# Kernel tuning notes

Measured on AMD Instinct MI355X. Metric: run time of the kernel, lower is better.

## Reference

```python
import jax, jax.numpy as jnp
import numpy as np

EMBED_DIM = 768
NUM_HEADS = 12
HEAD_DIM = EMBED_DIM // NUM_HEADS
B, L = 1, 2048


def setup_inputs() -> dict:
    key = jax.random.key(0)
    ks = jax.random.split(key, 10)
    D = EMBED_DIM
    s = 1.0 / np.sqrt(D)
    x = jax.random.normal(ks[0], (B, L, D), dtype=jnp.float32)
    Wq = jax.random.uniform(ks[1], (D, D), jnp.float32, -s, s)
    bq = jax.random.uniform(ks[2], (D,), jnp.float32, -s, s)
    Wk = jax.random.uniform(ks[3], (D, D), jnp.float32, -s, s)
    bk = jax.random.uniform(ks[4], (D,), jnp.float32, -s, s)
    Wv = jax.random.uniform(ks[5], (D, D), jnp.float32, -s, s)
    bv = jax.random.uniform(ks[6], (D,), jnp.float32, -s, s)
    Wo = jax.random.uniform(ks[7], (D, D), jnp.float32, -s, s)
    bo = jax.random.uniform(ks[8], (D,), jnp.float32, -s, s)
    theta = jnp.zeros((1, NUM_HEADS, 1, 1), dtype=jnp.float32)
    return {"x": x, "Wq": Wq, "bq": bq, "Wk": Wk, "bk": bk,
            "Wv": Wv, "bv": bv, "Wo": Wo, "bo": bo, "theta": theta}


def _heads(t):
    # [B,L,D] -> [B,H,L,d_k]
    b, l, d = t.shape
    return t.reshape(b, l, NUM_HEADS, HEAD_DIM).transpose(0, 2, 1, 3)


def reference(x, Wq, bq, Wk, bk, Wv, bv, Wo, bo, theta):
    b, l, d = x.shape
    d_k = HEAD_DIM
    q = _heads(x @ Wq.T + bq)  # [B,H,L,dk]
    k = _heads(x @ Wk.T + bk)
    v = _heads(x @ Wv.T + bv)
    # squared pairwise L2 distance (== torch.cdist(q,k,p=2)**2), scaled by d_k
    qn = jnp.sum(q * q, axis=-1, keepdims=True)          # [B,H,L,1]
    kn = jnp.sum(k * k, axis=-1, keepdims=True)          # [B,H,L,1]
    qk = jnp.einsum('bhid,bhjd->bhij', q, k)             # [B,H,L,L]
    dist_sq = jnp.maximum(qn + kn.transpose(0, 1, 3, 2) - 2.0 * qk, 0.0) / d_k
    # global max over the full LxL matrix per (B,H)
    dist_max = jnp.max(dist_sq, axis=(-1, -2), keepdims=True)
    dist_norm = dist_sq / (dist_max + 1e-6)
    dsexp = jnp.exp(theta)                               # [1,H,1,1]
    attn_logits = jnp.exp(-dsexp * dist_norm)            # [B,H,L,L]
    attn_weights = jax.nn.softmax(attn_logits, axis=-1)
    context = jnp.einsum('bhij,bhjd->bhid', attn_weights, v)  # [B,H,L,dk]
    context = context.transpose(0, 2, 1, 3).reshape(b, l, d)
    output = context @ Wo.T + bo
    return output, attn_weights.mean(axis=1)
```

## Files before the change

kernel.cpp:

```cpp
#include <hip/hip_runtime.h>
#include <hip/hip_bf16.h>


typedef __bf16 bf16_t;
typedef bf16_t bf16x8 __attribute__((ext_vector_type(8)));
typedef bf16_t bf16x4 __attribute__((ext_vector_type(4)));
typedef float f32x4 __attribute__((ext_vector_type(4)));

#define L_SEQ 2048
#define DIM 768
#define NH 12
#define DKH 64
#define MDJ 4

__device__ __forceinline__ bf16x8 ldg8(const bf16_t* p) { return *(const bf16x8*)p; }
__device__ __forceinline__ f32x4 mfma16(bf16x8 a, bf16x8 b, f32x4 c_) {
  return __builtin_amdgcn_mfma_f32_16x16x32_bf16(a, b, c_, 0, 0, 0);
}


struct Tile2 { bf16x8 r[2]; };

__device__ __forceinline__ void tile_load(const bf16_t* __restrict__ src, int stride,
                                          Tile2& t_, int tid) {
#pragma unroll
  for (int c = 0; c < 2; ++c) {
    int chunk = tid + c * 256;
    t_.r[c] = *(const bf16x8*)&src[(size_t)(chunk >> 3) * stride + (chunk & 7) * 8];
  }
}

__device__ __forceinline__ void tile_write(bf16_t (*dst)[72], const Tile2& t_, int tid) {
#pragma unroll
  for (int c = 0; c < 2; ++c) {
    int chunk = tid + c * 256;
    *(bf16x8*)&dst[chunk >> 3][(chunk & 7) * 8] = t_.r[c];
  }
}

__device__ __forceinline__ void mfma_nt64(bf16_t (*As)[72], bf16_t (*Bs)[72],
                                          int wid, int lane, f32x4 acc[4]) {
#pragma unroll
  for (int ks = 0; ks < 2; ++ks) {
    bf16x8 a = *(const bf16x8*)&As[wid * 16 + (lane & 15)][ks * 32 + (lane >> 4) * 8];
#pragma unroll
    for (int nt = 0; nt < 4; ++nt) {
      bf16x8 b = *(const bf16x8*)&Bs[nt * 16 + (lane & 15)][ks * 32 + (lane >> 4) * 8];
      acc[nt] = mfma16(a, b, acc[nt]);
    }
  }
}


__global__ void cast_x(const float* __restrict__ in, bf16_t* __restrict__ out, int n4) {
  int i = blockIdx.x * 256 + threadIdx.x;
  if (i >= n4) return;
  float4 v = ((const float4*)in)[i];
  bf16_t* o = out + (size_t)i * 4;
  o[0] = (bf16_t)v.x; o[1] = (bf16_t)v.y; o[2] = (bf16_t)v.z; o[3] = (bf16_t)v.w;
}

__global__ void cast_w4(const float* __restrict__ w0, const float* __restrict__ w1,
                        const float* __restrict__ w2, const float* __restrict__ w3,
                        bf16_t* __restrict__ o0, bf16_t* __restrict__ o1,
                        bf16_t* __restrict__ o2, bf16_t* __restrict__ o3, int n4) {
  int i = blockIdx.x * 256 + threadIdx.x;
  if (i >= n4) return;
  const float* in = blockIdx.y == 0 ? w0 : blockIdx.y == 1 ? w1 : blockIdx.y == 2 ? w2 : w3;
  bf16_t* out = blockIdx.y == 0 ? o0 : blockIdx.y == 1 ? o1 : blockIdx.y == 2 ? o2 : o3;
  float4 v = ((const float4*)in)[i];
  bf16_t* o = out + (size_t)i * 4;
  o[0] = (bf16_t)v.x; o[1] = (bf16_t)v.y; o[2] = (bf16_t)v.z; o[3] = (bf16_t)v.w;
}


__global__ __launch_bounds__(256) void gemm_qkv(const bf16_t* __restrict__ x,
                                                const bf16_t* __restrict__ Bq,
                                                const bf16_t* __restrict__ Bk,
                                                const bf16_t* __restrict__ Bv,
                                                const float* __restrict__ bq,
                                                const float* __restrict__ bk,
                                                const float* __restrict__ bv,
                                                bf16_t* __restrict__ qo,
                                                bf16_t* __restrict__ ko,
                                                bf16_t* __restrict__ vto,
                                                float* __restrict__ qn,
                                                float* __restrict__ kn) {
  __shared__ bf16_t As[2][64][72];
  __shared__ bf16_t Bs[2][64][72];
  const int z = blockIdx.z;
  const bf16_t* B = z == 0 ? Bq : z == 1 ? Bk : Bv;
  const float* bias = z == 0 ? bq : z == 1 ? bk : bv;
  const int tid = threadIdx.x, wid = tid >> 6, lane = tid & 63;
  const int c = lane & 15, hi = lane >> 4;
  const int m0 = blockIdx.y * 64, n0 = blockIdx.x * 64;
  Tile2 at, bt;
  tile_load(x + (size_t)m0 * DIM, DIM, at, tid);
  tile_load(B + (size_t)n0 * DIM, DIM, bt, tid);
  f32x4 acc[4] = {};
  for (int kk = 0; kk < 12; ++kk) {
    tile_write(As[kk & 1], at, tid);
    tile_write(Bs[kk & 1], bt, tid);
    __syncthreads();
    if (kk < 11) {
      tile_load(x + (size_t)m0 * DIM + (kk + 1) * 64, DIM, at, tid);
      tile_load(B + (size_t)n0 * DIM + (kk + 1) * 64, DIM, bt, tid);
    }
    mfma_nt64(As[kk & 1], Bs[kk & 1], wid, lane, acc);
    __syncthreads();
  }
  const int r0 = wid * 16 + hi * 4;
  float ss[4] = {0.f, 0.f, 0.f, 0.f};
#pragma unroll
  for (int nt = 0; nt < 4; ++nt) {
    int cc = n0 + nt * 16 + c;
    float bv_ = bias[cc];
    int h = cc >> 6, d = cc & 63;
#pragma unroll
    for (int r = 0; r < 4; ++r) {
      int mm = m0 + r0 + r;
      float val = acc[nt][r] + bv_;
      if (z == 2) {
        vto[(size_t)cc * L_SEQ + mm] = (bf16_t)val;
      } else {
        bf16_t* out = z == 0 ? qo : ko;
        out[((size_t)h * L_SEQ + mm) * 64 + d] = (bf16_t)val;
        ss[r] = fmaf(val, val, ss[r]);
      }
    }
  }
  if (z < 2) {
#pragma unroll
    for (int s = 1; s < 16; s <<= 1)
#pragma unroll
      for (int r = 0; r < 4; ++r) ss[r] += __shfl_xor(ss[r], s);
    if (c == 0) {
      float* norm = z == 0 ? qn : kn;
      int h = n0 >> 6;
#pragma unroll
      for (int r = 0; r < 4; ++r) norm[h * L_SEQ + m0 + r0 + r] = ss[r];
    }
  }
}

__global__ __launch_bounds__(256) void gemm_out(const bf16_t* __restrict__ A,
                                                const bf16_t* __restrict__ B,
                                                const float* __restrict__ bias,
                                                float* __restrict__ out) {
  __shared__ bf16_t As[2][64][72];
  __shared__ bf16_t Bs[2][64][72];
  const int tid = threadIdx.x, wid = tid >> 6, lane = tid & 63;
  const int c = lane & 15, hi = lane >> 4;
  const int m0 = blockIdx.y * 64, n0 = blockIdx.x * 64;
  Tile2 at, bt;
  tile_load(A + (size_t)m0 * DIM, DIM, at, tid);
  tile_load(B + (size_t)n0 * DIM, DIM, bt, tid);
  f32x4 acc[4] = {};
  for (int kk = 0; kk < 12; ++kk) {
    tile_write(As[kk & 1], at, tid);
    tile_write(Bs[kk & 1], bt, tid);
    __syncthreads();
    if (kk < 11) {
      tile_load(A + (size_t)m0 * DIM + (kk + 1) * 64, DIM, at, tid);
      tile_load(B + (size_t)n0 * DIM + (kk + 1) * 64, DIM, bt, tid);
    }
    mfma_nt64(As[kk & 1], Bs[kk & 1], wid, lane, acc);
    __syncthreads();
  }
  const int r0 = wid * 16 + hi * 4;
#pragma unroll
  for (int nt = 0; nt < 4; ++nt) {
    int cc = n0 + nt * 16 + c;
    float bv = bias[cc];
#pragma unroll
    for (int r = 0; r < 4; ++r)
      out[(size_t)(m0 + r0 + r) * DIM + cc] = acc[nt][r] + bv;
  }
}


__global__ __launch_bounds__(256) void maxdist(const bf16_t* __restrict__ q,
                                               const bf16_t* __restrict__ k,
                                               const float* __restrict__ qn,
                                               const float* __restrict__ kn,
                                               float* __restrict__ blockmax) {
  __shared__ bf16_t Ks[2][64][72];
  __shared__ float wmax[4];
  const int it = blockIdx.x, jc = blockIdx.y, h = blockIdx.z;
  const int i0 = it * 64, jbase = jc * (L_SEQ / MDJ);
  const int tid = threadIdx.x, wid = tid >> 6, lane = tid & 63;
  const int c = lane & 15, hi = lane >> 4;
  bf16x8 qb[4][2];
  float aq[4];
#pragma unroll
  for (int nt = 0; nt < 4; ++nt) {
    const bf16_t* qr = q + ((size_t)h * L_SEQ + i0 + nt * 16 + c) * DKH;
    qb[nt][0] = ldg8(qr + hi * 8);
    qb[nt][1] = ldg8(qr + 32 + hi * 8);
    aq[nt] = qn[h * L_SEQ + i0 + nt * 16 + c];
  }
  Tile2 kt;
  tile_load(k + ((size_t)h * L_SEQ + jbase) * DKH, DKH, kt, tid);
  float m = 0.f;
  const int NT = L_SEQ / MDJ / 64;
  for (int t = 0; t < NT; ++t) {
    tile_write(Ks[t & 1], kt, tid);
    if (t < NT - 1)
      tile_load(k + ((size_t)h * L_SEQ + jbase + (t + 1) * 64) * DKH, DKH, kt, tid);
    __syncthreads();
    f32x4 acc[4] = {};
#pragma unroll
    for (int ks = 0; ks < 2; ++ks) {
      bf16x8 a = *(const bf16x8*)&Ks[t & 1][wid * 16 + c][ks * 32 + hi * 8];
#pragma unroll
      for (int nt = 0; nt < 4; ++nt) acc[nt] = mfma16(a, qb[nt][ks], acc[nt]);
    }
    f32x4 knj = *(const f32x4*)&kn[h * L_SEQ + jbase + t * 64 + wid * 16 + hi * 4];
#pragma unroll
    for (int nt = 0; nt < 4; ++nt)
#pragma unroll
      for (int r = 0; r < 4; ++r)
        m = fmaxf(m, fmaf(-2.f, acc[nt][r], aq[nt] + knj[r]));
  }
#pragma unroll
  for (int s = 1; s < 64; s <<= 1) m = fmaxf(m, __shfl_xor(m, s));
  if (lane == 0) wmax[wid] = m;
  __syncthreads();
  if (tid == 0) {
    float bm = fmaxf(fmaxf(wmax[0], wmax[1]), fmaxf(wmax[2], wmax[3]));
    blockmax[(h * MDJ + jc) * (L_SEQ / 64) + it] = fmaxf(bm, 0.f) * (1.f / 64.f);
  }
}

__global__ void reduce_dmax(const float* __restrict__ blockmax, float* __restrict__ dmax) {
  __shared__ float wm[2];
  const int h = blockIdx.x, tid = threadIdx.x, lane = tid & 63, wid = tid >> 6;
  float m = blockmax[h * 128 + tid];
#pragma unroll
  for (int s = 1; s < 64; s <<= 1) m = fmaxf(m, __shfl_xor(m, s));
  if (lane == 0) wm[wid] = m;
  __syncthreads();
  if (tid == 0) dmax[h] = fmaxf(wm[0], wm[1]);
}


__global__ __launch_bounds__(256) void fusedctx(const bf16_t* __restrict__ q,
                                                const bf16_t* __restrict__ k,
                                                const bf16_t* __restrict__ vt,
                                                const float* __restrict__ qn,
                                                const float* __restrict__ kn,
                                                const float* __restrict__ dmax,
                                                const float* __restrict__ theta,
                                                float* __restrict__ denP,
                                                float* __restrict__ ctxP, int JC) {
  __shared__ bf16_t Ks[2][64][72];
  __shared__ bf16_t Vs[2][64][72];
  __shared__ bf16_t Ws[64][72];
  __shared__ float denW[4][64];
  const int it = blockIdx.x, jc = blockIdx.y, h = blockIdx.z;
  const int i0 = it * 64;
  const int JLEN = L_SEQ / JC, jbase = jc * JLEN;
  const int tid = threadIdx.x, wid = tid >> 6, lane = tid & 63;
  const int c = lane & 15, hi = lane >> 4;
  const float sc = __expf(theta[h]) * (1.f / 64.f) / (dmax[h] + 1e-6f);
  const float twosc = 2.f * sc;
  bf16x8 qb[4][2];
  float naq[4];
#pragma unroll
  for (int nt = 0; nt < 4; ++nt) {
    const bf16_t* qr = q + ((size_t)h * L_SEQ + i0 + nt * 16 + c) * DKH;
    qb[nt][0] = ldg8(qr + hi * 8);
    qb[nt][1] = ldg8(qr + 32 + hi * 8);
    naq[nt] = -sc * qn[h * L_SEQ + i0 + nt * 16 + c];
  }
  Tile2 kt, vtr;
  tile_load(k + ((size_t)h * L_SEQ + jbase) * DKH, DKH, kt, tid);
  tile_load(vt + (size_t)h * DKH * L_SEQ + jbase, L_SEQ, vtr, tid);
  float psum[4] = {0.f, 0.f, 0.f, 0.f};
  f32x4 cacc[4] = {};
  const int NT = JLEN / 64;
  for (int t = 0; t < NT; ++t) {
    tile_write(Ks[t & 1], kt, tid);
    tile_write(Vs[t & 1], vtr, tid);
    if (t < NT - 1) {
      tile_load(k + ((size_t)h * L_SEQ + jbase + (t + 1) * 64) * DKH, DKH, kt, tid);
      tile_load(vt + (size_t)h * DKH * L_SEQ + jbase + (t + 1) * 64, L_SEQ, vtr, tid);
    }
    __syncthreads();
    f32x4 acc[4] = {};
#pragma unroll
    for (int ks = 0; ks < 2; ++ks) {
      bf16x8 a = *(const bf16x8*)&Ks[t & 1][wid * 16 + c][ks * 32 + hi * 8];
#pragma unroll
      for (int nt = 0; nt < 4; ++nt) acc[nt] = mfma16(a, qb[nt][ks], acc[nt]);
    }
    f32x4 knj = *(const f32x4*)&kn[h * L_SEQ + jbase + t * 64 + wid * 16 + hi * 4];
    f32x4 sknj = knj * sc;
#pragma unroll
    for (int nt = 0; nt < 4; ++nt) {
      bf16x4 wp;
#pragma unroll
      for (int r = 0; r < 4; ++r) {
        float tt = fminf(fmaf(twosc, acc[nt][r], naq[nt] - sknj[r]), 0.f);
        float w = __expf(__expf(tt));
        psum[nt] += w;
        wp[r] = (bf16_t)w;
      }
      *(bf16x4*)&Ws[nt * 16 + c][wid * 16 + hi * 4] = wp;
    }
    __syncthreads();
#pragma unroll
    for (int ks = 0; ks < 2; ++ks) {
      bf16x8 a = *(const bf16x8*)&Vs[t & 1][wid * 16 + c][ks * 32 + hi * 8];
#pragma unroll
      for (int nt = 0; nt < 4; ++nt) {
        bf16x8 b = *(const bf16x8*)&Ws[nt * 16 + c][ks * 32 + hi * 8];
        cacc[nt] = mfma16(a, b, cacc[nt]);
      }
    }
  }
#pragma unroll
  for (int nt = 0; nt < 4; ++nt) {
    psum[nt] += __shfl_xor(psum[nt], 16);
    psum[nt] += __shfl_xor(psum[nt], 32);
  }
  if (lane < 16)
#pragma unroll
    for (int nt = 0; nt < 4; ++nt) denW[wid][nt * 16 + lane] = psum[nt];
  __syncthreads();
  if (tid < 64)
    denP[(size_t)(h * JC + jc) * L_SEQ + i0 + tid] =
        denW[0][tid] + denW[1][tid] + denW[2][tid] + denW[3][tid];
  float* P = ctxP + ((size_t)(h * JC + jc) * 32 + it) * 4096;
#pragma unroll
  for (int nt = 0; nt < 4; ++nt)
    *(f32x4*)&P[(nt * 16 + c) * 64 + wid * 16 + hi * 4] = cacc[nt];
}

__global__ __launch_bounds__(256) void ctx_combine(const float* __restrict__ denP,
                                                   const float* __restrict__ ctxP,
                                                   float* __restrict__ den,
                                                   bf16_t* __restrict__ ctx, int JC) {
  __shared__ float invL[64];
  const int it = blockIdx.x, h = blockIdx.y, tid = threadIdx.x;
  const int i0 = it * 64;
  if (tid < 64) {
    float d0 = 0.f;
    for (int jc = 0; jc < JC; ++jc)
      d0 += denP[(size_t)(h * JC + jc) * L_SEQ + i0 + tid];
    den[h * L_SEQ + i0 + tid] = d0;
    invL[tid] = 1.f / d0;
  }
  __syncthreads();
  const int il = tid >> 2, db = (tid & 3) * 16;
  const float inv = invL[il];
  bf16_t* dst = ctx + (size_t)(i0 + il) * DIM + h * 64 + db;
#pragma unroll
  for (int half = 0; half < 2; ++half) {
    bf16x8 o;
#pragma unroll
    for (int e = 0; e < 2; ++e) {
      f32x4 v = {0.f, 0.f, 0.f, 0.f};
      for (int jc = 0; jc < JC; ++jc)
        v += *(const f32x4*)&ctxP[((size_t)(h * JC + jc) * 32 + it) * 4096 +
                                  il * 64 + db + half * 8 + e * 4];
#pragma unroll
      for (int j = 0; j < 4; ++j) o[e * 4 + j] = (bf16_t)(v[j] * inv);
    }
    *(bf16x8*)&dst[half * 8] = o;
  }
}

__global__ __launch_bounds__(256) void attnmean(const bf16_t* __restrict__ q,
                                                const bf16_t* __restrict__ k,
                                                const float* __restrict__ qn,
                                                const float* __restrict__ kn,
                                                const float* __restrict__ dmax,
                                                const float* __restrict__ theta,
                                                const float* __restrict__ den,
                                                float* __restrict__ out1) {
  __shared__ bf16_t Qs[2][64][72];
  __shared__ bf16_t Ks[2][64][72];
  const int j0 = blockIdx.x * 64, i0 = blockIdx.y * 64;
  const int tid = threadIdx.x, wid = tid >> 6, lane = tid & 63;
  const int c = lane & 15, hi = lane >> 4;
  Tile2 qt, kt;
  tile_load(q + (size_t)i0 * DKH, DKH, qt, tid);
  tile_load(k + (size_t)j0 * DKH, DKH, kt, tid);
  f32x4 macc[4] = {};
  for (int h = 0; h < NH; ++h) {
    const int b = h & 1;
    tile_write(Qs[b], qt, tid);
    tile_write(Ks[b], kt, tid);
    __syncthreads();
    if (h < NH - 1) {
      tile_load(q + ((size_t)(h + 1) * L_SEQ + i0) * DKH, DKH, qt, tid);
      tile_load(k + ((size_t)(h + 1) * L_SEQ + j0) * DKH, DKH, kt, tid);
    }
    const float sc = __expf(theta[h]) * (1.f / 64.f) / (dmax[h] + 1e-6f);
    const float twosc = 2.f * sc;
    f32x4 acc[4] = {};
#pragma unroll
    for (int ks = 0; ks < 2; ++ks) {
      bf16x8 a = *(const bf16x8*)&Ks[b][wid * 16 + c][ks * 32 + hi * 8];
#pragma unroll
      for (int nt = 0; nt < 4; ++nt) {
        bf16x8 bq_ = *(const bf16x8*)&Qs[b][nt * 16 + c][ks * 32 + hi * 8];
        acc[nt] = mfma16(a, bq_, acc[nt]);
      }
    }
    f32x4 knj = *(const f32x4*)&kn[h * L_SEQ + j0 + wid * 16 + hi * 4];
    f32x4 sknj = knj * sc;
#pragma unroll
    for (int nt = 0; nt < 4; ++nt) {
      float naq = -sc * qn[h * L_SEQ + i0 + nt * 16 + c];
      float inv = 1.f / den[h * L_SEQ + i0 + nt * 16 + c];
#pragma unroll
      for (int r = 0; r < 4; ++r) {
        float tt = fminf(fmaf(twosc, acc[nt][r], naq - sknj[r]), 0.f);
        float w = __expf(__expf(tt));
        macc[nt][r] = fmaf(w, inv, macc[nt][r]);
      }
    }
    __syncthreads();
  }
#pragma unroll
  for (int nt = 0; nt < 4; ++nt) {
    f32x4 o = macc[nt] * (1.f / 12.f);
    *(f32x4*)&out1[(size_t)(i0 + nt * 16 + c) * L_SEQ + j0 + wid * 16 + hi * 4] = o;
  }
}


extern "C" void kernel_launch(void* const* d_in, const int* in_sizes, int n_in,
                              void* d_out, int out_size, void* d_ws, size_t ws_size,
                              hipStream_t stream) {
  const float* x = (const float*)d_in[0];
  const float* Wq = (const float*)d_in[1];
  const float* bq = (const float*)d_in[2];
  const float* Wk = (const float*)d_in[3];
  const float* bk = (const float*)d_in[4];
  const float* Wv = (const float*)d_in[5];
  const float* bv = (const float*)d_in[6];
  const float* Wo = (const float*)d_in[7];
  const float* bo = (const float*)d_in[8];
  const float* theta = (const float*)d_in[9];

  bf16_t* x_bf = (bf16_t*)d_ws;
  bf16_t* Wq_bf = x_bf + (size_t)L_SEQ * DIM;
  bf16_t* Wk_bf = Wq_bf + (size_t)DIM * DIM;
  bf16_t* Wv_bf = Wk_bf + (size_t)DIM * DIM;
  bf16_t* Wo_bf = Wv_bf + (size_t)DIM * DIM;
  bf16_t* q_bf = Wo_bf + (size_t)DIM * DIM;
  bf16_t* k_bf = q_bf + (size_t)NH * L_SEQ * DKH;
  bf16_t* vt_bf = k_bf + (size_t)NH * L_SEQ * DKH;
  bf16_t* ctx_bf = vt_bf + (size_t)NH * L_SEQ * DKH;
  float* qn = (float*)(ctx_bf + (size_t)L_SEQ * DIM);
  float* kn = qn + NH * L_SEQ;
  float* den = kn + NH * L_SEQ;
  float* dmax = den + NH * L_SEQ;
  float* blockmax = dmax + 64;
  float* denP = blockmax + 2048;
  float* ctxP = denP + 4 * NH * L_SEQ;

  size_t fixed_bytes = (size_t)((char*)ctxP - (char*)d_ws);
  int JC = (fixed_bytes + (size_t)4 * NH * 32 * 4096 * 4 <= ws_size) ? 4 : 2;

  float* out0 = (float*)d_out;
  float* out1 = out0 + (size_t)L_SEQ * DIM;

  cast_x<<<(L_SEQ * DIM / 4 + 255) / 256, 256, 0, stream>>>(x, x_bf, L_SEQ * DIM / 4);
  cast_w4<<<dim3((DIM * DIM / 4 + 255) / 256, 4), 256, 0, stream>>>(
      Wq, Wk, Wv, Wo, Wq_bf, Wk_bf, Wv_bf, Wo_bf, DIM * DIM / 4);

  gemm_qkv<<<dim3(DIM / 64, L_SEQ / 64, 3), 256, 0, stream>>>(
      x_bf, Wq_bf, Wk_bf, Wv_bf, bq, bk, bv, q_bf, k_bf, vt_bf, qn, kn);

  maxdist<<<dim3(L_SEQ / 64, MDJ, NH), 256, 0, stream>>>(q_bf, k_bf, qn, kn, blockmax);
  reduce_dmax<<<NH, 128, 0, stream>>>(blockmax, dmax);

  fusedctx<<<dim3(L_SEQ / 64, JC, NH), 256, 0, stream>>>(q_bf, k_bf, vt_bf, qn, kn,
                                                         dmax, theta, denP, ctxP, JC);
  ctx_combine<<<dim3(L_SEQ / 64, NH), 256, 0, stream>>>(denP, ctxP, den, ctx_bf, JC);

  attnmean<<<dim3(L_SEQ / 64, L_SEQ / 64), 256, 0, stream>>>(q_bf, k_bf, qn, kn, dmax,
                                                             theta, den, out1);
  gemm_out<<<dim3(DIM / 64, L_SEQ / 64), 256, 0, stream>>>(ctx_bf, Wo_bf, bo, out0);
}
```

Baseline: 142.2 us.

## Use 128x128 tiled GEMM template for QKV and output projections; switch exp to exp2

Replaces the two 64x64-tile projection GEMMs with one templated 128x128-tile kernel that uses dynamic shared memory, where each wave computes a 32x128 sub-tile. The larger tile raises reuse of each shared-memory load per MFMA, but it cuts the grid to 6x16 blocks per GEMM, which may underfill the GPU. Separately, the double-exponential weight in fusedctx and attnmean is rewritten with exp2f and log2e prescaling to save a multiply per exponential. A small cleanup ties the reduce_dmax size to MDJ.

```diff
diff --git a/kernel.cpp b/kernel.cpp
--- a/kernel.cpp
+++ b/kernel.cpp
@@ -12,6 +12,7 @@
 #define NH 12
 #define DKH 64
 #define MDJ 4
+#define L2E 1.44269504f
 
 __device__ __forceinline__ bf16x8 ldg8(const bf16_t* p) { return *(const bf16x8*)p; }
 __device__ __forceinline__ f32x4 mfma16(bf16x8 a, bf16x8 b, f32x4 c_) {
@@ -38,16 +39,24 @@
   }
 }
 
-__device__ __forceinline__ void mfma_nt64(bf16_t (*As)[72], bf16_t (*Bs)[72],
-                                          int wid, int lane, f32x4 acc[4]) {
-#pragma unroll
-  for (int ks = 0; ks < 2; ++ks) {
-    bf16x8 a = *(const bf16x8*)&As[wid * 16 + (lane & 15)][ks * 32 + (lane >> 4) * 8];
-#pragma unroll
-    for (int nt = 0; nt < 4; ++nt) {
-      bf16x8 b = *(const bf16x8*)&Bs[nt * 16 + (lane & 15)][ks * 32 + (lane >> 4) * 8];
-      acc[nt] = mfma16(a, b, acc[nt]);
-    }
+
+struct Tile4 { bf16x8 r[4]; };
+
+__device__ __forceinline__ void tile_load4(const bf16_t* __restrict__ src, int stride,
+                                           Tile4& t_, int tid) {
+#pragma unroll
+  for (int c = 0; c < 4; ++c) {
+    int chunk = tid + c * 256;
+    t_.r[c] = *(const bf16x8*)&src[(size_t)(chunk >> 3) * stride + (chunk & 7) * 8];
+  }
+}
+
+__device__ __forceinline__ void tile_write4(bf16_t* __restrict__ dst, const Tile4& t_,
+                                            int tid) {
+#pragma unroll
+  for (int c = 0; c < 4; ++c) {
+    int chunk = tid + c * 256;
+    *(bf16x8*)&dst[(chunk >> 3) * 72 + (chunk & 7) * 8] = t_.r[c];
   }
 }
 
@@ -73,108 +82,100 @@
   o[0] = (bf16_t)v.x; o[1] = (bf16_t)v.y; o[2] = (bf16_t)v.z; o[3] = (bf16_t)v.w;
 }
 
-
-__global__ __launch_bounds__(256) void gemm_qkv(const bf16_t* __restrict__ x,
-                                                const bf16_t* __restrict__ Bq,
-                                                const bf16_t* __restrict__ Bk,
-                                                const bf16_t* __restrict__ Bv,
-                                                const float* __restrict__ bq,
-                                                const float* __restrict__ bk,
-                                                const float* __restrict__ bv,
-                                                bf16_t* __restrict__ qo,
-                                                bf16_t* __restrict__ ko,
-                                                bf16_t* __restrict__ vto,
-                                                float* __restrict__ qn,
-                                                float* __restrict__ kn) {
-  __shared__ bf16_t As[2][64][72];
-  __shared__ bf16_t Bs[2][64][72];
-  const int z = blockIdx.z;
-  const bf16_t* B = z == 0 ? Bq : z == 1 ? Bk : Bv;
-  const float* bias = z == 0 ? bq : z == 1 ? bk : bv;
+template <int MODE>
+__global__ __launch_bounds__(256, 2) void gemm128(const bf16_t* __restrict__ A,
+                                                  const bf16_t* __restrict__ Bq,
+                                                  const bf16_t* __restrict__ Bk,
+                                                  const bf16_t* __restrict__ Bv,
+                                                  const float* __restrict__ bq,
+                                                  const float* __restrict__ bk,
+                                                  const float* __restrict__ bv,
+                                                  bf16_t* __restrict__ qo,
+                                                  bf16_t* __restrict__ ko,
+                                                  bf16_t* __restrict__ vto,
+                                                  float* __restrict__ outf,
+                                                  float* __restrict__ qn,
+                                                  float* __restrict__ kn) {
+  extern __shared__ bf16_t smem[];
+  const int z = MODE == 0 ? blockIdx.z : 0;
+  const bf16_t* B = MODE == 1 ? Bq : (z == 0 ? Bq : z == 1 ? Bk : Bv);
+  const float* bias = MODE == 1 ? bq : (z == 0 ? bq : z == 1 ? bk : bv);
   const int tid = threadIdx.x, wid = tid >> 6, lane = tid & 63;
   const int c = lane & 15, hi = lane >> 4;
-  const int m0 = blockIdx.y * 64, n0 = blockIdx.x * 64;
-  Tile2 at, bt;
-  tile_load(x + (size_t)m0 * DIM, DIM, at, tid);
-  tile_load(B + (size_t)n0 * DIM, DIM, bt, tid);
-  f32x4 acc[4] = {};
+  const int m0 = blockIdx.y * 128, n0 = blockIdx.x * 128;
+  Tile4 at, bt;
+  tile_load4(A + (size_t)m0 * DIM, DIM, at, tid);
+  tile_load4(B + (size_t)n0 * DIM, DIM, bt, tid);
+  f32x4 acc[2][8] = {};
   for (int kk = 0; kk < 12; ++kk) {
-    tile_write(As[kk & 1], at, tid);
-    tile_write(Bs[kk & 1], bt, tid);
+    bf16_t* Ab = smem + (kk & 1) * (128 * 72);
+    bf16_t* Bb = smem + 2 * (128 * 72) + (kk & 1) * (128 * 72);
+    tile_write4(Ab, at, tid);
+    tile_write4(Bb, bt, tid);
     __syncthreads();
     if (kk < 11) {
-      tile_load(x + (size_t)m0 * DIM + (kk + 1) * 64, DIM, at, tid);
-      tile_load(B + (size_t)n0 * DIM + (kk + 1) * 64, DIM, bt, tid);
-    }
-    mfma_nt64(As[kk & 1], Bs[kk & 1], wid, lane, acc);
-    __syncthreads();
-  }
-  const int r0 = wid * 16 + hi * 4;
-  float ss[4] = {0.f, 0.f, 0.f, 0.f};
-#pragma unroll
-  for (int nt = 0; nt < 4; ++nt) {
-    int cc = n0 + nt * 16 + c;
+      tile_load4(A + (size_t)m0 * DIM + (kk + 1) * 64, DIM, at, tid);
+      tile_load4(B + (size_t)n0 * DIM + (kk + 1) * 64, DIM, bt, tid);
+    }
+#pragma unroll
+    for (int ks = 0; ks < 2; ++ks) {
+      bf16x8 a0 = *(const bf16x8*)&Ab[(wid * 32 + c) * 72 + ks * 32 + hi * 8];
+      bf16x8 a1 = *(const bf16x8*)&Ab[(wid * 32 + 16 + c) * 72 + ks * 32 + hi * 8];
+#pragma unroll
+      for (int nf = 0; nf < 8; ++nf) {
+        bf16x8 b = *(const bf16x8*)&Bb[(nf * 16 + c) * 72 + ks * 32 + hi * 8];
+        acc[0][nf] = mfma16(a0, b, acc[0][nf]);
+        acc[1][nf] = mfma16(a1, b, acc[1][nf]);
+      }
+    }
+    __syncthreads();
+  }
+  float ss[2][4][2] = {};
+#pragma unroll
+  for (int nf = 0; nf < 8; ++nf) {
+    int cc = n0 + nf * 16 + c;
     float bv_ = bias[cc];
     int h = cc >> 6, d = cc & 63;
 #pragma unroll
-    for (int r = 0; r < 4; ++r) {
-      int mm = m0 + r0 + r;
-      float val = acc[nt][r] + bv_;
-      if (z == 2) {
-        vto[(size_t)cc * L_SEQ + mm] = (bf16_t)val;
-      } else {
-        bf16_t* out = z == 0 ? qo : ko;
-        out[((size_t)h * L_SEQ + mm) * 64 + d] = (bf16_t)val;
-        ss[r] = fmaf(val, val, ss[r]);
-      }
-    }
-  }
-  if (z < 2) {
+    for (int mf = 0; mf < 2; ++mf) {
+#pragma unroll
+      for (int r = 0; r < 4; ++r) {
+        int mm = m0 + wid * 32 + mf * 16 + hi * 4 + r;
+        float val = acc[mf][nf][r] + bv_;
+        if (MODE == 1) {
+          outf[(size_t)mm * DIM + cc] = val;
+        } else if (z == 2) {
+          vto[(size_t)cc * L_SEQ + mm] = (bf16_t)val;
+        } else {
+          bf16_t* out = z == 0 ? qo : ko;
+          out[((size_t)h * L_SEQ + mm) * 64 + d] = (bf16_t)val;
+          ss[mf][r][nf >> 2] = fmaf(val, val, ss[mf][r][nf >> 2]);
+        }
+      }
+    }
+  }
+  if (MODE == 0 && z < 2) {
 #pragma unroll
     for (int s = 1; s < 16; s <<= 1)
 #pragma unroll
-      for (int r = 0; r < 4; ++r) ss[r] += __shfl_xor(ss[r], s);
+      for (int mf = 0; mf < 2; ++mf)
+#pragma unroll
+        for (int r = 0; r < 4; ++r) {
+          ss[mf][r][0] += __shfl_xor(ss[mf][r][0], s);
+          ss[mf][r][1] += __shfl_xor(ss[mf][r][1], s);
+        }
     if (c == 0) {
       float* norm = z == 0 ? qn : kn;
-      int h = n0 >> 6;
-#pragma unroll
-      for (int r = 0; r < 4; ++r) norm[h * L_SEQ + m0 + r0 + r] = ss[r];
-    }
-  }
-}
-
-__global__ __launch_bounds__(256) void gemm_out(const bf16_t* __restrict__ A,
-                                                const bf16_t* __restrict__ B,
-                                                const float* __restrict__ bias,
-                                                float* __restrict__ out) {
-  __shared__ bf16_t As[2][64][72];
-  __shared__ bf16_t Bs[2][64][72];
-  const int tid = threadIdx.x, wid = tid >> 6, lane = tid & 63;
-  const int c = lane & 15, hi = lane >> 4;
-  const int m0 = blockIdx.y * 64, n0 = blockIdx.x * 64;
-  Tile2 at, bt;
-  tile_load(A + (size_t)m0 * DIM, DIM, at, tid);
-  tile_load(B + (size_t)n0 * DIM, DIM, bt, tid);
-  f32x4 acc[4] = {};
-  for (int kk = 0; kk < 12; ++kk) {
-    tile_write(As[kk & 1], at, tid);
-    tile_write(Bs[kk & 1], bt, tid);
-    __syncthreads();
-    if (kk < 11) {
-      tile_load(A + (size_t)m0 * DIM + (kk + 1) * 64, DIM, at, tid);
-      tile_load(B + (size_t)n0 * DIM + (kk + 1) * 64, DIM, bt, tid);
-    }
-    mfma_nt64(As[kk & 1], Bs[kk & 1], wid, lane, acc);
-    __syncthreads();
-  }
-  const int r0 = wid * 16 + hi * 4;
-#pragma unroll
-  for (int nt = 0; nt < 4; ++nt) {
-    int cc = n0 + nt * 16 + c;
-    float bv = bias[cc];
-#pragma unroll
-    for (int r = 0; r < 4; ++r)
-      out[(size_t)(m0 + r0 + r) * DIM + cc] = acc[nt][r] + bv;
+#pragma unroll
+      for (int hh = 0; hh < 2; ++hh) {
+        int h = (n0 >> 6) + hh;
+#pragma unroll
+        for (int mf = 0; mf < 2; ++mf)
+#pragma unroll
+          for (int r = 0; r < 4; ++r)
+            norm[h * L_SEQ + m0 + wid * 32 + mf * 16 + hi * 4 + r] = ss[mf][r][hh];
+      }
+    }
   }
 }
 
@@ -235,7 +236,7 @@
 __global__ void reduce_dmax(const float* __restrict__ blockmax, float* __restrict__ dmax) {
   __shared__ float wm[2];
   const int h = blockIdx.x, tid = threadIdx.x, lane = tid & 63, wid = tid >> 6;
-  float m = blockmax[h * 128 + tid];
+  float m = blockmax[h * (MDJ * 32) + tid];
 #pragma unroll
   for (int s = 1; s < 64; s <<= 1) m = fmaxf(m, __shfl_xor(m, s));
   if (lane == 0) wm[wid] = m;
@@ -263,7 +264,8 @@
   const int tid = threadIdx.x, wid = tid >> 6, lane = tid & 63;
   const int c = lane & 15, hi = lane >> 4;
   const float sc = __expf(theta[h]) * (1.f / 64.f) / (dmax[h] + 1e-6f);
-  const float twosc = 2.f * sc;
+  const float scl = sc * L2E;
+  const float twoscl = 2.f * scl;
   bf16x8 qb[4][2];
   float naq[4];
 #pragma unroll
@@ -271,7 +273,7 @@
     const bf16_t* qr = q + ((size_t)h * L_SEQ + i0 + nt * 16 + c) * DKH;
     qb[nt][0] = ldg8(qr + hi * 8);
     qb[nt][1] = ldg8(qr + 32 + hi * 8);
-    naq[nt] = -sc * qn[h * L_SEQ + i0 + nt * 16 + c];
+    naq[nt] = -scl * qn[h * L_SEQ + i0 + nt * 16 + c];
   }
   Tile2 kt, vtr;
   tile_load(k + ((size_t)h * L_SEQ + jbase) * DKH, DKH, kt, tid);
@@ -295,14 +297,14 @@
       for (int nt = 0; nt < 4; ++nt) acc[nt] = mfma16(a, qb[nt][ks], acc[nt]);
     }
     f32x4 knj = *(const f32x4*)&kn[h * L_SEQ + jbase + t * 64 + wid * 16 + hi * 4];
-    f32x4 sknj = knj * sc;
+    f32x4 sknj = knj * scl;
 #pragma unroll
     for (int nt = 0; nt < 4; ++nt) {
       bf16x4 wp;
 #pragma unroll
       for (int r = 0; r < 4; ++r) {
-        float tt = fminf(fmaf(twosc, acc[nt][r], naq[nt] - sknj[r]), 0.f);
-        float w = __expf(__expf(tt));
+        float ttl = fminf(fmaf(twoscl, acc[nt][r], naq[nt] - sknj[r]), 0.f);
+        float w = exp2f(exp2f(ttl) * L2E);
         psum[nt] += w;
         wp[r] = (bf16_t)w;
       }
@@ -370,6 +372,7 @@
     *(bf16x8*)&dst[half * 8] = o;
   }
 }
+
 
 __global__ __launch_bounds__(256) void attnmean(const bf16_t* __restrict__ q,
                                                 const bf16_t* __restrict__ k,
@@ -398,7 +401,8 @@
       tile_load(k + ((size_t)(h + 1) * L_SEQ + j0) * DKH, DKH, kt, tid);
     }
     const float sc = __expf(theta[h]) * (1.f / 64.f) / (dmax[h] + 1e-6f);
-    const float twosc = 2.f * sc;
+    const float scl = sc * L2E;
+    const float twoscl = 2.f * scl;
     f32x4 acc[4] = {};
 #pragma unroll
     for (int ks = 0; ks < 2; ++ks) {
@@ -410,15 +414,15 @@
       }
     }
     f32x4 knj = *(const f32x4*)&kn[h * L_SEQ + j0 + wid * 16 + hi * 4];
-    f32x4 sknj = knj * sc;
+    f32x4 sknj = knj * scl;
 #pragma unroll
     for (int nt = 0; nt < 4; ++nt) {
-      float naq = -sc * qn[h * L_SEQ + i0 + nt * 16 + c];
+      float naq = -scl * qn[h * L_SEQ + i0 + nt * 16 + c];
       float inv = 1.f / den[h * L_SEQ + i0 + nt * 16 + c];
 #pragma unroll
       for (int r = 0; r < 4; ++r) {
-        float tt = fminf(fmaf(twosc, acc[nt][r], naq - sknj[r]), 0.f);
-        float w = __expf(__expf(tt));
+        float ttl = fminf(fmaf(twoscl, acc[nt][r], naq - sknj[r]), 0.f);
+        float w = exp2f(exp2f(ttl) * L2E);
         macc[nt][r] = fmaf(w, inv, macc[nt][r]);
       }
     }
@@ -473,11 +477,12 @@
   cast_w4<<<dim3((DIM * DIM / 4 + 255) / 256, 4), 256, 0, stream>>>(
       Wq, Wk, Wv, Wo, Wq_bf, Wk_bf, Wv_bf, Wo_bf, DIM * DIM / 4);
 
-  gemm_qkv<<<dim3(DIM / 64, L_SEQ / 64, 3), 256, 0, stream>>>(
-      x_bf, Wq_bf, Wk_bf, Wv_bf, bq, bk, bv, q_bf, k_bf, vt_bf, qn, kn);
+  const size_t shmem = (size_t)4 * 128 * 72 * sizeof(bf16_t);
+  gemm128<0><<<dim3(DIM / 128, L_SEQ / 128, 3), 256, shmem, stream>>>(
+      x_bf, Wq_bf, Wk_bf, Wv_bf, bq, bk, bv, q_bf, k_bf, vt_bf, nullptr, qn, kn);
 
   maxdist<<<dim3(L_SEQ / 64, MDJ, NH), 256, 0, stream>>>(q_bf, k_bf, qn, kn, blockmax);
-  reduce_dmax<<<NH, 128, 0, stream>>>(blockmax, dmax);
+  reduce_dmax<<<NH, MDJ * 32, 0, stream>>>(blockmax, dmax);
 
   fusedctx<<<dim3(L_SEQ / 64, JC, NH), 256, 0, stream>>>(q_bf, k_bf, vt_bf, qn, kn,
                                                          dmax, theta, denP, ctxP, JC);
@@ -485,5 +490,7 @@
 
   attnmean<<<dim3(L_SEQ / 64, L_SEQ / 64), 256, 0, stream>>>(q_bf, k_bf, qn, kn, dmax,
                                                              theta, den, out1);
-  gemm_out<<<dim3(DIM / 64, L_SEQ / 64), 256, 0, stream>>>(ctx_bf, Wo_bf, bo, out0);
-}
+  gemm128<1><<<dim3(DIM / 128, L_SEQ / 128), 256, shmem, stream>>>(
+      ctx_bf, Wo_bf, nullptr, nullptr, bo, nullptr, nullptr,
+      nullptr, nullptr, nullptr, out0, nullptr, nullptr);
+}
```

New measurement: 169.4 us. 1.19x slower.
